# Kernel optimization log

Hardware: AMD Instinct MI355X
Metric: run time of the kernel (lower is better)

## Reference

```python
import jax, jax.numpy as jnp
import numpy as np

EPS = 1e-6


def setup_inputs() -> dict:
    key = jax.random.key(0)
    kx, kp = jax.random.split(key)
    B, D, P = 16384, 1024, 1024
    x = jax.random.normal(kx, (B, D), dtype=jnp.float32)
    prototypes = jax.random.normal(kp, (P, D), dtype=jnp.float32)
    return {"x": x, "prototypes": prototypes}


def reference(x, prototypes):
    # Vectorized form of the per-(sample, prototype) yat similarity:
    #   score[i, j] = <x_i, p_j>^2 / (||x_i - p_j||^2 + eps)
    # x: [B, D], prototypes: [P, D] -> scores: [B, P]
    x_flat = x.reshape(x.shape[0], -1)
    dots = jnp.einsum("bd,pd->bp", x_flat, prototypes)          # [B, P] GEMM
    x_sq = jnp.sum(x_flat * x_flat, axis=-1, keepdims=True)      # [B, 1]
    p_sq = jnp.sum(prototypes * prototypes, axis=-1)[None, :]    # [1, P]
    dist_sq = x_sq + p_sq - 2.0 * dots                            # ||x - p||^2
    scores = (dots * dots) / (dist_sq + EPS)
    return scores.astype(jnp.float32)
```

## Files before the change

### kernel.cpp

```cpp
#include <hip/hip_runtime.h>
#include <hip/hip_bf16.h>

#define EPS 1e-6f

typedef __attribute__((ext_vector_type(8))) __bf16 bf16x8;
typedef __attribute__((ext_vector_type(4))) float f32x4;

__global__ __launch_bounds__(512, 4) void yat_fused(
    const float* __restrict__ X, const float* __restrict__ Pr,
    float* __restrict__ out, int M, int N, int K) {

    __shared__ __align__(128) char sm[65536];
    __shared__ __align__(16) float sqx[128];
    __shared__ __align__(16) float sqp[128];
    const char* smc = (const char*)sm;

    const int t = threadIdx.x;
    const int lane = t & 63;
    const int wid = t >> 6;
    const int wm = wid >> 1;
    const int wn = wid & 1;

    const int nbx = N >> 7;
    const int nby = M >> 7;
    const int total = nbx * nby;
    int bid = blockIdx.x;
    bid = (bid & 7) * (total >> 3) + (bid >> 3);
    const int by = bid / nbx;
    const int bx = bid - by * nbx;
    const int brow = by << 7;
    const int bcol = bx << 7;

    const int NKT = K >> 6;

    f32x4 acc[2][4];
#pragma unroll
    for (int i = 0; i < 2; ++i)
#pragma unroll
        for (int j = 0; j < 4; ++j) acc[i][j] = (f32x4){0.f, 0.f, 0.f, 0.f};

    const int arow = lane & 15;
    const int kq16 = (lane >> 4) * 16;

    const int rsub = lane >> 3;
    const int lcq = (lane & 7) ^ rsub;
    const long baseA = (long)(brow + wid * 8 + rsub) * K + lcq * 8;
    const long baseB = (long)(bcol + wid * 8 + rsub) * K + lcq * 8;
    const long sL = (long)64 * K;
    const int dlane = wid * 1024 + lane * 16;

    f32x4 c0[2], c1[2];
    float qA[2] = {0.f, 0.f};
    float qB[2] = {0.f, 0.f};

#define ISSUE(buf, G, BASE, s, kt) do {                                        \
    const float* g0_ = (G) + BASE + (s) * sL + (long)(kt) * 64;                \
    buf[0] = *(const f32x4*)(g0_);                                             \
    buf[1] = *(const f32x4*)(g0_ + 4);                                         \
} while (0)

#define WRITE(buf, Q, s, slot, boff) do {                                      \
    f32x4 u_ = buf[0], v_ = buf[1];                                            \
    Q[s] += u_[0]*u_[0] + u_[1]*u_[1] + u_[2]*u_[2] + u_[3]*u_[3]              \
          + v_[0]*v_[0] + v_[1]*v_[1] + v_[2]*v_[2] + v_[3]*v_[3];             \
    bf16x8 pk_;                                                                \
    _Pragma("unroll")                                                          \
    for (int i_ = 0; i_ < 4; ++i_) {                                           \
        pk_[i_]     = (__bf16)u_[i_];                                          \
        pk_[4 + i_] = (__bf16)v_[i_];                                          \
    }                                                                          \
    *(bf16x8*)((char*)sm + (slot) * 32768 + (boff) + (s) * 8192 + dlane) = pk_;\
} while (0)

#define READ_A(slot) do {                                                      \
    _Pragma("unroll")                                                          \
    for (int mi_ = 0; mi_ < 2; ++mi_) {                                        \
        int r_ = wm * 32 + mi_ * 16 + arow;                                    \
        const char* p_ = smc + (slot) * 32768 + r_ * 128;                      \
        int s_ = (r_ & 7) << 4;                                                \
        af[mi_][0] = *(const bf16x8*)(p_ + (kq16 ^ s_));                       \
        af[mi_][1] = *(const bf16x8*)(p_ + ((64 + kq16) ^ s_));                \
    }                                                                          \
} while (0)

#define READ_B(slot, nh, dst) do {                                             \
    _Pragma("unroll")                                                          \
    for (int ni_ = 0; ni_ < 2; ++ni_) {                                        \
        int r_ = wn * 64 + (nh) * 32 + ni_ * 16 + arow;                        \
        const char* p_ = smc + (slot) * 32768 + 16384 + r_ * 128;              \
        int s_ = (r_ & 7) << 4;                                                \
        dst[ni_][0] = *(const bf16x8*)(p_ + (kq16 ^ s_));                      \
        dst[ni_][1] = *(const bf16x8*)(p_ + ((64 + kq16) ^ s_));               \
    }                                                                          \
} while (0)

#define MFMA_H(nh, bset) do {                                                  \
    __builtin_amdgcn_s_setprio(1);                                             \
    _Pragma("unroll")                                                          \
    for (int kk_ = 0; kk_ < 2; ++kk_)                                          \
        _Pragma("unroll")                                                      \
        for (int mi_ = 0; mi_ < 2; ++mi_)                                      \
            _Pragma("unroll")                                                  \
            for (int ni_ = 0; ni_ < 2; ++ni_)                                  \
                acc[mi_][(nh) * 2 + ni_] =                                     \
                    __builtin_amdgcn_mfma_f32_16x16x32_bf16(                   \
                        af[mi_][kk_], bset[ni_][kk_],                          \
                        acc[mi_][(nh) * 2 + ni_], 0, 0, 0);                    \
    __builtin_amdgcn_s_setprio(0);                                             \
} while (0)

#define PBAR() do {                                                            \
    __builtin_amdgcn_s_barrier();                                              \
    __builtin_amdgcn_sched_barrier(0);                                         \
    asm volatile("" ::: "memory");                                             \
} while (0)
#define LGKMDRAIN() asm volatile("s_waitcnt lgkmcnt(0)" ::: "memory")

    bf16x8 af[2][2];
    bf16x8 bf0[2][2], bf1[2][2];

    ISSUE(c0, X, baseA, 0, 0);
    ISSUE(c1, X, baseA, 1, 0);
    WRITE(c0, qA, 0, 0, 0);       ISSUE(c0, Pr, baseB, 0, 0);
    WRITE(c1, qA, 1, 0, 0);       ISSUE(c1, Pr, baseB, 1, 0);
    WRITE(c0, qB, 0, 0, 16384);
    WRITE(c1, qB, 1, 0, 16384);
    if (NKT > 1) { ISSUE(c0, X, baseA, 0, 1); ISSUE(c1, X, baseA, 1, 1); }
    LGKMDRAIN();
    PBAR();

    for (int kt = 0; kt < NKT; ++kt) {
        const int slot = kt & 1;
        const int nslot = slot ^ 1;
        const bool more = (kt + 1) < NKT;
        const bool more2 = (kt + 2) < NKT;

        if (more) {
            WRITE(c0, qA, 0, nslot, 0);      ISSUE(c0, Pr, baseB, 0, kt + 1);
            WRITE(c1, qA, 1, nslot, 0);      ISSUE(c1, Pr, baseB, 1, kt + 1);
        }
        READ_A(slot); READ_B(slot, 0, bf0);
        MFMA_H(0, bf0); PBAR();
        if (more) {
            WRITE(c0, qB, 0, nslot, 16384);
            WRITE(c1, qB, 1, nslot, 16384);
        }
        if (more2) { ISSUE(c0, X, baseA, 0, kt + 2); ISSUE(c1, X, baseA, 1, kt + 2); }
        READ_B(slot, 1, bf1);
        MFMA_H(1, bf1);
        LGKMDRAIN();
        PBAR();
    }

#undef ISSUE
#undef WRITE
#undef READ_A
#undef READ_B
#undef MFMA_H
#undef PBAR
#undef LGKMDRAIN

#pragma unroll
    for (int s = 0; s < 2; ++s) {
        float a = qA[s], b = qB[s];
#pragma unroll
        for (int m = 1; m <= 4; m <<= 1) {
            a += __shfl_xor(a, m);
            b += __shfl_xor(b, m);
        }
        if ((lane & 7) == 0) {
            int r = s * 64 + wid * 8 + rsub;
            sqx[r] = a;
            sqp[r] = b;
        }
    }
    __syncthreads();

    float* smf = (float*)sm;
#pragma unroll
    for (int ni = 0; ni < 4; ++ni) {
        int lcc = wn * 64 + ni * 16 + arow;
        float ps = sqp[lcc];
#pragma unroll
        for (int mi = 0; mi < 2; ++mi) {
            f32x4 c = acc[mi][ni];
            int lr0 = wm * 32 + mi * 16 + (lane >> 4) * 4;
            f32x4 xs4 = *(const f32x4*)(&sqx[lr0]);
            int lcs = lcc ^ (((lr0 >> 2) & 1) << 4);
#pragma unroll
            for (int j = 0; j < 4; ++j) {
                float dv = c[j];
                float denom = xs4[j] + ps - 2.0f * dv + EPS;
                smf[(lr0 + j) * 128 + lcs] = dv * dv / denom;
            }
        }
    }
    __syncthreads();
#pragma unroll
    for (int it = 0; it < 8; ++it) {
        int r = it * 16 + (t >> 5);
        int swz = ((r >> 2) & 1) << 4;
        int c0l = (t & 31) * 4;
        f32x4 v = *(const f32x4*)(smf + r * 128 + (c0l ^ swz));
        *(f32x4*)(out + (size_t)(brow + r) * N + bcol + c0l) = v;
    }
}

__global__ void yat_fallback(const float* __restrict__ x, const float* __restrict__ p,
                             float* __restrict__ out, int B, int P, int D) {
    __shared__ float xs[1024];
    int b = blockIdx.x;
    int pc = blockIdx.y * 256 + threadIdx.x;
    for (int i = threadIdx.x; i < D; i += 256) xs[i] = x[(size_t)b * D + i];
    __syncthreads();
    if (pc >= P) return;
    float dot = 0.f, psq = 0.f, xsq = 0.f;
    for (int k = 0; k < D; ++k) {
        float pv = p[(size_t)pc * D + k];
        float xv = xs[k];
        dot += xv * pv;
        psq += pv * pv;
        xsq += xv * xv;
    }
    float denom = xsq + psq - 2.f * dot + EPS;
    out[(size_t)b * P + pc] = dot * dot / denom;
}

extern "C" void kernel_launch(void* const* d_in, const int* in_sizes, int n_in,
                              void* d_out, int out_size, void* d_ws, size_t ws_size,
                              hipStream_t stream) {
    const float* x = (const float*)d_in[0];
    const float* p = (const float*)d_in[1];
    float* out = (float*)d_out;

    const int D = 1024;
    const int B = in_sizes[0] / D;
    const int P = in_sizes[1] / D;

    int nblocks = (B / 128) * (P / 128);
    if ((B % 128) || (P % 128) || (D % 64) || (nblocks % 8)) {
        yat_fallback<<<dim3(B, (P + 255) / 256), 256, 0, stream>>>(x, p, out, B, P, D);
        return;
    }

    yat_fused<<<dim3(nblocks), 512, 0, stream>>>(x, p, out, B, P, D);
}
```

Measured before the change: 72.34 us.

## Enlarge block tile to 256x256 with 16 waves and 4x4 per-wave MFMA tiles

Doubles the output tile per workgroup from 128x128 to 256x256, using 1024 threads (16 waves in a 4x4 grid), each computing a 64x64 sub-tile with 4x4 MFMA accumulators. LDS grows to 128KB double-buffered, and the epilogue is split into two passes of 128 rows so the staging buffer fits. The aim is higher arithmetic intensity and fewer global reloads of X and prototypes, since each tile is reused across more outputs. The trade-offs are more registers per wave, only one workgroup per CU given the LDS size, and fewer blocks (256) to spread across the CUs.

```diff
diff --git a/kernel.cpp b/kernel.cpp
--- a/kernel.cpp
+++ b/kernel.cpp
@@ -6,36 +6,36 @@
 typedef __attribute__((ext_vector_type(8))) __bf16 bf16x8;
 typedef __attribute__((ext_vector_type(4))) float f32x4;
 
-__global__ __launch_bounds__(512, 4) void yat_fused(
+__global__ __launch_bounds__(1024, 4) void yat_fused(
     const float* __restrict__ X, const float* __restrict__ Pr,
     float* __restrict__ out, int M, int N, int K) {
 
-    __shared__ __align__(128) char sm[65536];
-    __shared__ __align__(16) float sqx[128];
-    __shared__ __align__(16) float sqp[128];
+    __shared__ __align__(128) char sm[131072];
+    __shared__ __align__(16) float sqx[256];
+    __shared__ __align__(16) float sqp[256];
     const char* smc = (const char*)sm;
 
     const int t = threadIdx.x;
     const int lane = t & 63;
     const int wid = t >> 6;
-    const int wm = wid >> 1;
-    const int wn = wid & 1;
-
-    const int nbx = N >> 7;
-    const int nby = M >> 7;
+    const int wr = wid >> 2;
+    const int wc = wid & 3;
+
+    const int nbx = N >> 8;
+    const int nby = M >> 8;
     const int total = nbx * nby;
     int bid = blockIdx.x;
     bid = (bid & 7) * (total >> 3) + (bid >> 3);
     const int by = bid / nbx;
     const int bx = bid - by * nbx;
-    const int brow = by << 7;
-    const int bcol = bx << 7;
+    const int brow = by << 8;
+    const int bcol = bx << 8;
 
     const int NKT = K >> 6;
 
-    f32x4 acc[2][4];
-#pragma unroll
-    for (int i = 0; i < 2; ++i)
+    f32x4 acc[4][4];
+#pragma unroll
+    for (int i = 0; i < 4; ++i)
 #pragma unroll
         for (int j = 0; j < 4; ++j) acc[i][j] = (f32x4){0.f, 0.f, 0.f, 0.f};
 
@@ -46,7 +46,7 @@
     const int lcq = (lane & 7) ^ rsub;
     const long baseA = (long)(brow + wid * 8 + rsub) * K + lcq * 8;
     const long baseB = (long)(bcol + wid * 8 + rsub) * K + lcq * 8;
-    const long sL = (long)64 * K;
+    const long sH = (long)128 * K;
     const int dlane = wid * 1024 + lane * 16;
 
     f32x4 c0[2], c1[2];
@@ -54,7 +54,7 @@
     float qB[2] = {0.f, 0.f};
 
 #define ISSUE(buf, G, BASE, s, kt) do {                                        \
-    const float* g0_ = (G) + BASE + (s) * sL + (long)(kt) * 64;                \
+    const float* g0_ = (G) + BASE + (s) * sH + (long)(kt) * 64;                \
     buf[0] = *(const f32x4*)(g0_);                                             \
     buf[1] = *(const f32x4*)(g0_ + 4);                                         \
 } while (0)
@@ -69,43 +69,37 @@
         pk_[i_]     = (__bf16)u_[i_];                                          \
         pk_[4 + i_] = (__bf16)v_[i_];                                          \
     }                                                                          \
-    *(bf16x8*)((char*)sm + (slot) * 32768 + (boff) + (s) * 8192 + dlane) = pk_;\
-} while (0)
-
-#define READ_A(slot) do {                                                      \
-    _Pragma("unroll")                                                          \
-    for (int mi_ = 0; mi_ < 2; ++mi_) {                                        \
-        int r_ = wm * 32 + mi_ * 16 + arow;                                    \
-        const char* p_ = smc + (slot) * 32768 + r_ * 128;                      \
+    *(bf16x8*)((char*)sm + (slot) * 65536 + (boff) + (s) * 16384 + dlane) = pk_;\
+} while (0)
+
+#define READ_A(slot, kk) do {                                                  \
+    _Pragma("unroll")                                                          \
+    for (int mi_ = 0; mi_ < 4; ++mi_) {                                        \
+        int r_ = wr * 64 + mi_ * 16 + arow;                                    \
+        const char* p_ = smc + (slot) * 65536 + r_ * 128;                      \
         int s_ = (r_ & 7) << 4;                                                \
-        af[mi_][0] = *(const bf16x8*)(p_ + (kq16 ^ s_));                       \
-        af[mi_][1] = *(const bf16x8*)(p_ + ((64 + kq16) ^ s_));                \
+        af[mi_] = *(const bf16x8*)(p_ + (((kk) * 64 + kq16) ^ s_));            \
     }                                                                          \
 } while (0)
 
-#define READ_B(slot, nh, dst) do {                                             \
-    _Pragma("unroll")                                                          \
-    for (int ni_ = 0; ni_ < 2; ++ni_) {                                        \
-        int r_ = wn * 64 + (nh) * 32 + ni_ * 16 + arow;                        \
-        const char* p_ = smc + (slot) * 32768 + 16384 + r_ * 128;              \
+#define READ_B(slot, kk) do {                                                  \
+    _Pragma("unroll")                                                          \
+    for (int ni_ = 0; ni_ < 4; ++ni_) {                                        \
+        int r_ = wc * 64 + ni_ * 16 + arow;                                    \
+        const char* p_ = smc + (slot) * 65536 + 32768 + r_ * 128;              \
         int s_ = (r_ & 7) << 4;                                                \
-        dst[ni_][0] = *(const bf16x8*)(p_ + (kq16 ^ s_));                      \
-        dst[ni_][1] = *(const bf16x8*)(p_ + ((64 + kq16) ^ s_));               \
+        bf[ni_] = *(const bf16x8*)(p_ + (((kk) * 64 + kq16) ^ s_));            \
     }                                                                          \
 } while (0)
 
-#define MFMA_H(nh, bset) do {                                                  \
+#define MFMA_S() do {                                                          \
     __builtin_amdgcn_s_setprio(1);                                             \
     _Pragma("unroll")                                                          \
-    for (int kk_ = 0; kk_ < 2; ++kk_)                                          \
+    for (int mi_ = 0; mi_ < 4; ++mi_)                                          \
         _Pragma("unroll")                                                      \
-        for (int mi_ = 0; mi_ < 2; ++mi_)                                      \
-            _Pragma("unroll")                                                  \
-            for (int ni_ = 0; ni_ < 2; ++ni_)                                  \
-                acc[mi_][(nh) * 2 + ni_] =                                     \
-                    __builtin_amdgcn_mfma_f32_16x16x32_bf16(                   \
-                        af[mi_][kk_], bset[ni_][kk_],                          \
-                        acc[mi_][(nh) * 2 + ni_], 0, 0, 0);                    \
+        for (int ni_ = 0; ni_ < 4; ++ni_)                                      \
+            acc[mi_][ni_] = __builtin_amdgcn_mfma_f32_16x16x32_bf16(           \
+                af[mi_], bf[ni_], acc[mi_][ni_], 0, 0, 0);                     \
     __builtin_amdgcn_s_setprio(0);                                             \
 } while (0)
 
@@ -116,15 +110,13 @@
 } while (0)
 #define LGKMDRAIN() asm volatile("s_waitcnt lgkmcnt(0)" ::: "memory")
 
-    bf16x8 af[2][2];
-    bf16x8 bf0[2][2], bf1[2][2];
-
-    ISSUE(c0, X, baseA, 0, 0);
-    ISSUE(c1, X, baseA, 1, 0);
-    WRITE(c0, qA, 0, 0, 0);       ISSUE(c0, Pr, baseB, 0, 0);
-    WRITE(c1, qA, 1, 0, 0);       ISSUE(c1, Pr, baseB, 1, 0);
-    WRITE(c0, qB, 0, 0, 16384);
-    WRITE(c1, qB, 1, 0, 16384);
+    bf16x8 af[4];
+    bf16x8 bf[4];
+
+    ISSUE(c0, X, baseA, 0, 0);  ISSUE(c1, X, baseA, 1, 0);
+    WRITE(c0, qA, 0, 0, 0);     WRITE(c1, qA, 1, 0, 0);
+    ISSUE(c0, Pr, baseB, 0, 0); ISSUE(c1, Pr, baseB, 1, 0);
+    WRITE(c0, qB, 0, 0, 32768); WRITE(c1, qB, 1, 0, 32768);
     if (NKT > 1) { ISSUE(c0, X, baseA, 0, 1); ISSUE(c1, X, baseA, 1, 1); }
     LGKMDRAIN();
     PBAR();
@@ -136,18 +128,18 @@
         const bool more2 = (kt + 2) < NKT;
 
         if (more) {
-            WRITE(c0, qA, 0, nslot, 0);      ISSUE(c0, Pr, baseB, 0, kt + 1);
-            WRITE(c1, qA, 1, nslot, 0);      ISSUE(c1, Pr, baseB, 1, kt + 1);
-        }
-        READ_A(slot); READ_B(slot, 0, bf0);
-        MFMA_H(0, bf0); PBAR();
+            WRITE(c0, qA, 0, nslot, 0);  ISSUE(c0, Pr, baseB, 0, kt + 1);
+            WRITE(c1, qA, 1, nslot, 0);  ISSUE(c1, Pr, baseB, 1, kt + 1);
+        }
+        READ_A(slot, 0); READ_B(slot, 0);
+        MFMA_S(); PBAR();
         if (more) {
-            WRITE(c0, qB, 0, nslot, 16384);
-            WRITE(c1, qB, 1, nslot, 16384);
+            WRITE(c0, qB, 0, nslot, 32768);
+            WRITE(c1, qB, 1, nslot, 32768);
         }
         if (more2) { ISSUE(c0, X, baseA, 0, kt + 2); ISSUE(c1, X, baseA, 1, kt + 2); }
-        READ_B(slot, 1, bf1);
-        MFMA_H(1, bf1);
+        READ_A(slot, 1); READ_B(slot, 1);
+        MFMA_S();
         LGKMDRAIN();
         PBAR();
     }
@@ -156,7 +148,7 @@
 #undef WRITE
 #undef READ_A
 #undef READ_B
-#undef MFMA_H
+#undef MFMA_S
 #undef PBAR
 #undef LGKMDRAIN
 
@@ -169,40 +161,46 @@
             b += __shfl_xor(b, m);
         }
         if ((lane & 7) == 0) {
-            int r = s * 64 + wid * 8 + rsub;
+            int r = s * 128 + wid * 8 + rsub;
             sqx[r] = a;
             sqp[r] = b;
         }
     }
-    __syncthreads();
 
     float* smf = (float*)sm;
 #pragma unroll
-    for (int ni = 0; ni < 4; ++ni) {
-        int lcc = wn * 64 + ni * 16 + arow;
-        float ps = sqp[lcc];
-#pragma unroll
-        for (int mi = 0; mi < 2; ++mi) {
-            f32x4 c = acc[mi][ni];
-            int lr0 = wm * 32 + mi * 16 + (lane >> 4) * 4;
-            f32x4 xs4 = *(const f32x4*)(&sqx[lr0]);
-            int lcs = lcc ^ (((lr0 >> 2) & 1) << 4);
-#pragma unroll
-            for (int j = 0; j < 4; ++j) {
-                float dv = c[j];
-                float denom = xs4[j] + ps - 2.0f * dv + EPS;
-                smf[(lr0 + j) * 128 + lcs] = dv * dv / denom;
+    for (int pass = 0; pass < 2; ++pass) {
+        __syncthreads();
+        if ((wr >> 1) == pass) {
+            const int wrl = wr & 1;
+#pragma unroll
+            for (int ni = 0; ni < 4; ++ni) {
+                int lcc = wc * 64 + ni * 16 + arow;
+                float ps = sqp[lcc];
+#pragma unroll
+                for (int mi = 0; mi < 4; ++mi) {
+                    f32x4 c = acc[mi][ni];
+                    int lr0 = wrl * 64 + mi * 16 + (lane >> 4) * 4;
+                    f32x4 xs4 = *(const f32x4*)(&sqx[pass * 128 + lr0]);
+                    int lcs = lcc ^ (((lr0 >> 2) & 1) << 4);
+#pragma unroll
+                    for (int j = 0; j < 4; ++j) {
+                        float dv = c[j];
+                        float denom = xs4[j] + ps - 2.0f * dv + EPS;
+                        smf[(lr0 + j) * 256 + lcs] = dv * dv / denom;
+                    }
+                }
             }
         }
-    }
-    __syncthreads();
-#pragma unroll
-    for (int it = 0; it < 8; ++it) {
-        int r = it * 16 + (t >> 5);
-        int swz = ((r >> 2) & 1) << 4;
-        int c0l = (t & 31) * 4;
-        f32x4 v = *(const f32x4*)(smf + r * 128 + (c0l ^ swz));
-        *(f32x4*)(out + (size_t)(brow + r) * N + bcol + c0l) = v;
+        __syncthreads();
+#pragma unroll
+        for (int it = 0; it < 8; ++it) {
+            int r = it * 16 + (t >> 6);
+            int swz = ((r >> 2) & 1) << 4;
+            int c0l = (t & 63) * 4;
+            f32x4 v = *(const f32x4*)(smf + r * 256 + (c0l ^ swz));
+            *(f32x4*)(out + (size_t)(brow + pass * 128 + r) * N + bcol + c0l) = v;
+        }
     }
 }
 
@@ -237,11 +235,11 @@
     const int B = in_sizes[0] / D;
     const int P = in_sizes[1] / D;
 
-    int nblocks = (B / 128) * (P / 128);
-    if ((B % 128) || (P % 128) || (D % 64) || (nblocks % 8)) {
+    int nblocks = (B / 256) * (P / 256);
+    if ((B % 256) || (P % 256) || (D % 64) || (nblocks % 8)) {
         yat_fallback<<<dim3(B, (P + 255) / 256), 256, 0, stream>>>(x, p, out, B, P, D);
         return;
     }
 
-    yat_fused<<<dim3(nblocks), 512, 0, stream>>>(x, p, out, B, P, D);
+    yat_fused<<<dim3(nblocks), 1024, 0, stream>>>(x, p, out, B, P, D);
 }
```

Measured after the change: 70.46 us. -2.6%, faster.
